# Kernel tuning notes

Measured on AMD Instinct MI355X. Metric: run time of the kernel, lower is better.

## Reference

```python
import jax, jax.numpy as jnp
import numpy as np

PAD_VALUE = 0.0


def setup_inputs() -> dict:
    key = jax.random.key(0)
    k1, k2 = jax.random.split(key)
    B, DIM, T = 16, 384, 512
    x = jax.random.normal(k1, (B, DIM, T), dtype=jnp.float32)
    duration = jax.random.randint(k2, (B, T), 0, 8, dtype=jnp.int32)
    return {"x": x, "duration": duration, "d_max": T * 8}


def reference(x, duration, d_max):
    """Length regulator (FastSpeech-style).

    x:        (B, dim, T) float32
    duration: (B, T) int32, frames per input timestep
    d_max:    static int, padded output frame length (>= max total duration)

    Returns:
      out:     (B, dim, d_max) expanded/padded tensor
      mel_len: (B,) int32 true output lengths
    """
    B, dim, T = x.shape
    # Guard against all-zero duration rows (original fills them with 1s).
    row_sum = duration.sum(axis=1)  # (B,)
    duration = jnp.where((row_sum == 0)[:, None], jnp.ones_like(duration), duration)

    cum = jnp.cumsum(duration, axis=1)  # (B, T) exclusive-end offsets
    mel_len = cum[:, -1]  # (B,)

    frames = jnp.arange(d_max, dtype=jnp.int32)  # (d_max,)
    # Source index for each output frame: first t with cum[t] > frame.
    idx = jax.vmap(lambda c: jnp.searchsorted(c, frames, side="right"))(cum)  # (B, d_max)
    idx = jnp.clip(idx, 0, T - 1)

    out = jnp.take_along_axis(x, idx[:, None, :], axis=2)  # (B, dim, d_max)
    valid = frames[None, :] < mel_len[:, None]  # (B, d_max)
    out = jnp.where(valid[:, None, :], out, jnp.asarray(PAD_VALUE, x.dtype))
    return out, mel_len
```

## Files before the change

### kernel.cpp

```cpp
#include <hip/hip_runtime.h>

#define B_SZ   16
#define DIM_SZ 384
#define T_SZ   512
#define DMAX   4096
#define DC     16
#define FC     1024

__global__ __launch_bounds__(T_SZ) void lr_scan_kernel(const int* __restrict__ duration,
                                                       int* __restrict__ ws_cum,
                                                       int* __restrict__ ws_mel,
                                                       float* __restrict__ mel_out) {
    __shared__ int buf[T_SZ];
    const int b = blockIdx.x;
    const int t = threadIdx.x;
    buf[t] = duration[b * T_SZ + t];
    __syncthreads();
    for (int off = 1; off < T_SZ; off <<= 1) {
        int v   = buf[t];
        int add = (t >= off) ? buf[t - off] : 0;
        __syncthreads();
        buf[t] = v + add;
        __syncthreads();
    }
    const int rowsum = buf[T_SZ - 1];
    const int cum = (rowsum == 0) ? (t + 1) : buf[t];
    ws_cum[b * T_SZ + t] = cum;
    if (t == T_SZ - 1) {
        const int ml = (rowsum == 0) ? T_SZ : rowsum;
        ws_mel[b] = ml;
        mel_out[b] = (float)ml;
    }
}

__global__ __launch_bounds__(256) void lr_gather_kernel(const float* __restrict__ x,
                                                        const int* __restrict__ ws_cum,
                                                        const int* __restrict__ ws_mel,
                                                        float* __restrict__ out) {
    __shared__ float s_x[DC * T_SZ];
    __shared__ int   s_cum[T_SZ];
    const int tid = threadIdx.x;
    const int b   = blockIdx.y;
    const int d0  = blockIdx.z * DC;
    const int f0  = blockIdx.x * FC;

    s_cum[tid]       = ws_cum[b * T_SZ + tid];
    s_cum[tid + 256] = ws_cum[b * T_SZ + tid + 256];

    const float4* __restrict__ xsrc = (const float4*)(x + ((size_t)b * DIM_SZ + d0) * T_SZ);
    float4* s_x4 = (float4*)s_x;
#pragma unroll
    for (int i = 0; i < (DC * T_SZ / 4) / 256; ++i)
        s_x4[i * 256 + tid] = xsrc[i * 256 + tid];
    __syncthreads();

    const int mel = ws_mel[b];
    const int f   = f0 + tid * 4;

    int  idx[4];
    bool valid[4];
#pragma unroll
    for (int j = 0; j < 4; ++j) {
        const int ff = f + j;
        int pos = 0;
#pragma unroll
        for (int step = 256; step > 0; step >>= 1) {
            if (s_cum[pos + step - 1] <= ff) pos += step;
        }
        idx[j]   = pos;
        valid[j] = (ff < mel);
    }

    float4* __restrict__ outp = (float4*)(out + (size_t)b * DIM_SZ * DMAX);
    const int f4 = (f0 >> 2) + tid;
#pragma unroll
    for (int dd = 0; dd < DC; ++dd) {
        const float* __restrict__ xr = s_x + dd * T_SZ;
        float4 v;
        v.x = valid[0] ? xr[idx[0]] : 0.0f;
        v.y = valid[1] ? xr[idx[1]] : 0.0f;
        v.z = valid[2] ? xr[idx[2]] : 0.0f;
        v.w = valid[3] ? xr[idx[3]] : 0.0f;
        outp[(size_t)(d0 + dd) * (DMAX / 4) + f4] = v;
    }
}

extern "C" void kernel_launch(void* const* d_in, const int* in_sizes, int n_in,
                              void* d_out, int out_size, void* d_ws, size_t ws_size,
                              hipStream_t stream) {
    const float* x        = (const float*)d_in[0];
    const int*   duration = (const int*)d_in[1];

    float* out     = (float*)d_out;
    float* mel_out = out + (size_t)B_SZ * DIM_SZ * DMAX;

    int* ws_cum = (int*)d_ws;
    int* ws_mel = ws_cum + B_SZ * T_SZ;

    lr_scan_kernel<<<B_SZ, T_SZ, 0, stream>>>(duration, ws_cum, ws_mel, mel_out);

    dim3 grid(DMAX / FC, B_SZ, DIM_SZ / DC);
    lr_gather_kernel<<<grid, 256, 0, stream>>>(x, ws_cum, ws_mel, out);
}
```

Before: 120.5 us.

## Use wave-level shuffle scan and skip search for padded frames in gather

The scan kernel becomes a single 64-lane wavefront: each lane loads eight durations with int4 loads and computes a local prefix, then a shuffle-up scan replaces the shared-memory scan with its many barriers. The gather kernel now covers two 1024-frame groups per block with half as many channels. Any frame group entirely past mel_len writes zeros directly and skips the binary search and shared-memory reads. The tile change halves the x staged per block and doubles how often each x tile is reused.

New measurement: 116.4 us. 1.04x faster.

```diff
diff --git a/kernel.cpp b/kernel.cpp
--- a/kernel.cpp
+++ b/kernel.cpp
@@ -4,29 +4,42 @@
 #define DIM_SZ 384
 #define T_SZ   512
 #define DMAX   4096
-#define DC     16
-#define FC     1024
+#define DC     8
+#define FC     2048
 
-__global__ __launch_bounds__(T_SZ) void lr_scan_kernel(const int* __restrict__ duration,
-                                                       int* __restrict__ ws_cum,
-                                                       int* __restrict__ ws_mel,
-                                                       float* __restrict__ mel_out) {
-    __shared__ int buf[T_SZ];
+__global__ __launch_bounds__(64) void lr_scan_kernel(const int* __restrict__ duration,
+                                                     int* __restrict__ ws_cum,
+                                                     int* __restrict__ ws_mel,
+                                                     float* __restrict__ mel_out) {
     const int b = blockIdx.x;
-    const int t = threadIdx.x;
-    buf[t] = duration[b * T_SZ + t];
-    __syncthreads();
-    for (int off = 1; off < T_SZ; off <<= 1) {
-        int v   = buf[t];
-        int add = (t >= off) ? buf[t - off] : 0;
-        __syncthreads();
-        buf[t] = v + add;
-        __syncthreads();
+    const int l = threadIdx.x;
+    const int4* __restrict__ src = (const int4*)(duration + b * T_SZ);
+    const int4 a = src[l * 2];
+    const int4 c = src[l * 2 + 1];
+    int p[8];
+    p[0] = a.x;        p[1] = p[0] + a.y; p[2] = p[1] + a.z; p[3] = p[2] + a.w;
+    p[4] = p[3] + c.x; p[5] = p[4] + c.y; p[6] = p[5] + c.z; p[7] = p[6] + c.w;
+    int s = p[7];
+#pragma unroll
+    for (int off = 1; off < 64; off <<= 1) {
+        const int v = __shfl_up(s, off);
+        if (l >= off) s += v;
     }
-    const int rowsum = buf[T_SZ - 1];
-    const int cum = (rowsum == 0) ? (t + 1) : buf[t];
-    ws_cum[b * T_SZ + t] = cum;
-    if (t == T_SZ - 1) {
+    const int excl   = s - p[7];
+    const int rowsum = __shfl(s, 63);
+    int4 o0, o1;
+    if (rowsum == 0) {
+        const int t0 = l * 8;
+        o0 = make_int4(t0 + 1, t0 + 2, t0 + 3, t0 + 4);
+        o1 = make_int4(t0 + 5, t0 + 6, t0 + 7, t0 + 8);
+    } else {
+        o0 = make_int4(excl + p[0], excl + p[1], excl + p[2], excl + p[3]);
+        o1 = make_int4(excl + p[4], excl + p[5], excl + p[6], excl + p[7]);
+    }
+    int4* __restrict__ dst = (int4*)(ws_cum + b * T_SZ);
+    dst[l * 2]     = o0;
+    dst[l * 2 + 1] = o1;
+    if (l == 63) {
         const int ml = (rowsum == 0) ? T_SZ : rowsum;
         ws_mel[b] = ml;
         mel_out[b] = (float)ml;
@@ -55,33 +68,42 @@
     __syncthreads();
 
     const int mel = ws_mel[b];
-    const int f   = f0 + tid * 4;
+    float4* __restrict__ outp = (float4*)(out + (size_t)b * DIM_SZ * DMAX);
 
-    int  idx[4];
-    bool valid[4];
 #pragma unroll
-    for (int j = 0; j < 4; ++j) {
-        const int ff = f + j;
-        int pos = 0;
+    for (int g = 0; g < FC / 1024; ++g) {
+        const int f  = f0 + g * 1024 + tid * 4;
+        const int f4 = f >> 2;
+        if (f >= mel) {
+            const float4 z = make_float4(0.f, 0.f, 0.f, 0.f);
 #pragma unroll
-        for (int step = 256; step > 0; step >>= 1) {
-            if (s_cum[pos + step - 1] <= ff) pos += step;
+            for (int dd = 0; dd < DC; ++dd)
+                outp[(size_t)(d0 + dd) * (DMAX / 4) + f4] = z;
+        } else {
+            int  idx[4];
+            bool valid[4];
+#pragma unroll
+            for (int j = 0; j < 4; ++j) {
+                const int ff = f + j;
+                int pos = 0;
+#pragma unroll
+                for (int step = 256; step > 0; step >>= 1) {
+                    if (s_cum[pos + step - 1] <= ff) pos += step;
+                }
+                idx[j]   = pos;
+                valid[j] = (ff < mel);
+            }
+#pragma unroll
+            for (int dd = 0; dd < DC; ++dd) {
+                const float* __restrict__ xr = s_x + dd * T_SZ;
+                float4 v;
+                v.x = valid[0] ? xr[idx[0]] : 0.0f;
+                v.y = valid[1] ? xr[idx[1]] : 0.0f;
+                v.z = valid[2] ? xr[idx[2]] : 0.0f;
+                v.w = valid[3] ? xr[idx[3]] : 0.0f;
+                outp[(size_t)(d0 + dd) * (DMAX / 4) + f4] = v;
+            }
         }
-        idx[j]   = pos;
-        valid[j] = (ff < mel);
-    }
-
-    float4* __restrict__ outp = (float4*)(out + (size_t)b * DIM_SZ * DMAX);
-    const int f4 = (f0 >> 2) + tid;
-#pragma unroll
-    for (int dd = 0; dd < DC; ++dd) {
-        const float* __restrict__ xr = s_x + dd * T_SZ;
-        float4 v;
-        v.x = valid[0] ? xr[idx[0]] : 0.0f;
-        v.y = valid[1] ? xr[idx[1]] : 0.0f;
-        v.z = valid[2] ? xr[idx[2]] : 0.0f;
-        v.w = valid[3] ? xr[idx[3]] : 0.0f;
-        outp[(size_t)(d0 + dd) * (DMAX / 4) + f4] = v;
     }
 }
 
@@ -97,7 +119,7 @@
     int* ws_cum = (int*)d_ws;
     int* ws_mel = ws_cum + B_SZ * T_SZ;
 
-    lr_scan_kernel<<<B_SZ, T_SZ, 0, stream>>>(duration, ws_cum, ws_mel, mel_out);
+    lr_scan_kernel<<<B_SZ, 64, 0, stream>>>(duration, ws_cum, ws_mel, mel_out);
 
     dim3 grid(DMAX / FC, B_SZ, DIM_SZ / DC);
     lr_gather_kernel<<<grid, 256, 0, stream>>>(x, ws_cum, ws_mel, out);
```
